# Kernel tuning notes

Hardware: AMD Instinct MI355X
Metric: run time of the kernel (lower is better)

Reference implementation:

```python
import jax, jax.numpy as jnp
import numpy as np

B, N, C, H, W = 4, 8, 256, 64, 64
SCALE = 2
D = C * SCALE  # embed_dim*scale, head_size with n_heads=1
EPS = 1e-6


def setup_inputs() -> dict:
    key = jax.random.key(0)
    ks = jax.random.split(key, 6)
    sc = lambda k, sh, f: jax.random.normal(k, sh, jnp.float32) * f
    return {
        "q": jax.random.normal(ks[0], (B, C), jnp.float32),
        "c": jax.random.normal(ks[1], (B, N, C, H, W), jnp.float32),
        "g": jnp.ones((C,), jnp.float32),                 # RMSNorm weight
        "Wq": sc(ks[2], (D, C), C ** -0.5),               # proj_q weight
        "Wkv": sc(ks[3], (2 * D, C), C ** -0.5),          # proj_kv weight
        "Wo": sc(ks[4], (C, D), D ** -0.5),               # proj_out weight
        "bo": jnp.zeros((C,), jnp.float32),               # proj_out bias
    }


def reference(q, c, g, Wq, Wkv, Wo, bo):
    # c: [B,N,C,H,W] -> [B,H,W,N,C]
    cp = jnp.transpose(c, (0, 3, 4, 1, 2))
    # RMSNorm over channel dim
    cn = cp * jax.lax.rsqrt(jnp.mean(cp * cp, axis=-1, keepdims=True) + EPS) * g
    # per-pixel, per-token k/v projection: [B,H,W,N,2D]
    kv = jnp.einsum('bhwnc,dc->bhwnd', cn, Wkv)
    k, v = jnp.split(kv, 2, axis=-1)                      # each [B,H,W,N,D]
    qp = q @ Wq.T                                         # [B,D]
    # broadcast single query over spatial grid; softmax over N context tokens
    dots = jnp.einsum('bd,bhwnd->bhwn', qp, k) * (D ** -0.5)
    att = jax.nn.softmax(dots, axis=-1)                   # [B,H,W,N]
    hvec = jnp.einsum('bhwn,bhwnd->bhwd', att, v)         # [B,H,W,D]
    out = hvec @ Wo.T + bo                                # [B,H,W,C]
    return jnp.transpose(out, (0, 3, 1, 2))               # [B,C,H,W]
```

## Files before the change

### kernel.cpp

```cpp
#include <hip/hip_runtime.h>


typedef __attribute__((ext_vector_type(8))) short short8;
typedef __attribute__((ext_vector_type(4))) float floatx4;

static __device__ __forceinline__ short f2bf(float f) {
  unsigned u = __float_as_uint(f);
  u += 0x7fffu + ((u >> 16) & 1u);
  return (short)(u >> 16);
}

__global__ __launch_bounds__(256) void pre_kernel(
    const float* __restrict__ q, const float* __restrict__ g,
    const float* __restrict__ Wq, const float* __restrict__ Wkv,
    const float* __restrict__ Wo, unsigned char* __restrict__ ws) {
  short* WovgB = (short*)ws;
  float* gqk = (float*)(ws + 131072);
  const int blk = blockIdx.x, tid = threadIdx.x;
  if (blk < 64) {
    const int i0 = blk * 4, c = tid;
    float s0 = 0.f, s1 = 0.f, s2 = 0.f, s3 = 0.f;
    #pragma unroll 8
    for (int d = 0; d < 512; ++d) {
      const float wv = Wkv[(512 + d) * 256 + c];
      s0 = fmaf(Wo[(i0 + 0) * 512 + d], wv, s0);
      s1 = fmaf(Wo[(i0 + 1) * 512 + d], wv, s1);
      s2 = fmaf(Wo[(i0 + 2) * 512 + d], wv, s2);
      s3 = fmaf(Wo[(i0 + 3) * 512 + d], wv, s3);
    }
    const float gc = g[c];
    const int sg = c >> 5, q2 = (c >> 3) & 3, jj = c & 7;
    const float sv[4] = {s0, s1, s2, s3};
    #pragma unroll
    for (int ii = 0; ii < 4; ++ii) {
      const int i = i0 + ii, it = i >> 4, m = i & 15;
      WovgB[((((it * 8 + sg) * 4 + q2) * 16) + m) * 8 + jj] = f2bf(sv[ii] * gc);
    }
  } else if (blk < 68) {
    const int b = blk - 64;
    __shared__ float qps[512];
    for (int d = tid; d < 512; d += 256) {
      float s = 0.f;
      #pragma unroll 16
      for (int cc = 0; cc < 256; ++cc)
        s = fmaf(Wq[d * 256 + cc], q[b * 256 + cc], s);
      qps[d] = s;
    }
    __syncthreads();
    const int c = tid;
    float s = 0.f;
    #pragma unroll 16
    for (int d = 0; d < 512; ++d)
      s = fmaf(Wkv[d * 256 + c], qps[d], s);
    gqk[b * 256 + c] = s * g[c] * 0.044194173824159216f;
  }
}

__global__ __launch_bounds__(512, 2) void attn_kernel(
    const float* __restrict__ cin, const float* __restrict__ bo,
    const unsigned char* __restrict__ ws, float* __restrict__ out) {
  const short8* Av = (const short8*)ws;
  const float* gqk = (const float*)(ws + 131072);
  const int blk = blockIdx.x;
  const int b = blk >> 6, h = blk & 63;
  const int tid = threadIdx.x;
  const int lane = tid & 63, w = tid >> 6;
  const int cgrp = tid >> 4;
  const int pgrp = tid & 15;

  __shared__ short tB[8][4][64][8];
  __shared__ float redS[2][8][16][4], redD[2][8][16][4];

  float rg[8];
  #pragma unroll
  for (int j = 0; j < 8; ++j) rg[j] = gqk[b * 256 + cgrp * 8 + j];

  float t[8][4];
  #pragma unroll
  for (int j = 0; j < 8; ++j)
    #pragma unroll
    for (int p = 0; p < 4; ++p) t[j][p] = 0.f;
  float mM[4], zZ[4];
  #pragma unroll
  for (int p = 0; p < 4; ++p) { mM[p] = -1e30f; zZ[p] = 0.f; }

  const float* cb = cin + ((size_t)(b * 8) * 256 + cgrp * 8) * 4096
                        + h * 64 + pgrp * 4;
  for (int n = 0; n < 8; ++n) {
    const float* cp = cb + (size_t)n * 256 * 4096;
    floatx4 vals[8];
    #pragma unroll
    for (int j = 0; j < 8; ++j)
      vals[j] = *(const floatx4*)(cp + (size_t)j * 4096);
    float ssq[4] = {0.f, 0.f, 0.f, 0.f}, dt[4] = {0.f, 0.f, 0.f, 0.f};
    #pragma unroll
    for (int j = 0; j < 8; ++j)
      #pragma unroll
      for (int p = 0; p < 4; ++p) {
        ssq[p] = fmaf(vals[j][p], vals[j][p], ssq[p]);
        dt[p] = fmaf(vals[j][p], rg[j], dt[p]);
      }
    #pragma unroll
    for (int p = 0; p < 4; ++p) {
      ssq[p] += __shfl_xor(ssq[p], 16);
      ssq[p] += __shfl_xor(ssq[p], 32);
      dt[p] += __shfl_xor(dt[p], 16);
      dt[p] += __shfl_xor(dt[p], 32);
    }
    if ((lane >> 4) == 0) {
      #pragma unroll
      for (int p = 0; p < 4; ++p) {
        redS[n & 1][w][pgrp][p] = ssq[p];
        redD[n & 1][w][pgrp][p] = dt[p];
      }
    }
    __syncthreads();
    floatx4 S = {0.f, 0.f, 0.f, 0.f}, Dt = {0.f, 0.f, 0.f, 0.f};
    #pragma unroll
    for (int ww = 0; ww < 8; ++ww) {
      S += *(const floatx4*)(&redS[n & 1][ww][pgrp][0]);
      Dt += *(const floatx4*)(&redD[n & 1][ww][pgrp][0]);
    }
    float wn[4], al[4];
    #pragma unroll
    for (int p = 0; p < 4; ++p) {
      const float invr = rsqrtf(S[p] * (1.f / 256.f) + 1e-6f);
      const float d = Dt[p] * invr;
      const float mn = fmaxf(mM[p], d);
      al[p] = __expf(mM[p] - mn);
      const float e = __expf(d - mn);
      zZ[p] = zZ[p] * al[p] + e;
      mM[p] = mn;
      wn[p] = e * invr;
    }
    #pragma unroll
    for (int j = 0; j < 8; ++j)
      #pragma unroll
      for (int p = 0; p < 4; ++p)
        t[j][p] = fmaf(wn[p], vals[j][p], t[j][p] * al[p]);
  }

  {
    const int s = cgrp >> 2, qq = cgrp & 3;
    const int nt = pgrp >> 2, mb = (pgrp & 3) * 4;
    #pragma unroll
    for (int p = 0; p < 4; ++p) {
      const float invZ = 1.f / zZ[p];
      short8 pk;
      #pragma unroll
      for (int j = 0; j < 8; ++j) pk[j] = f2bf(t[j][p] * invZ);
      *(short8*)(&tB[s][nt][qq * 16 + mb + p][0]) = pk;
    }
  }
  __syncthreads();

  const int qf = lane >> 4, m = lane & 15;
  floatx4 acc[2][4];
  #pragma unroll
  for (int mt = 0; mt < 2; ++mt)
    #pragma unroll
    for (int nt = 0; nt < 4; ++nt) acc[mt][nt] = (floatx4){0.f, 0.f, 0.f, 0.f};
  #pragma unroll
  for (int s = 0; s < 8; ++s) {
    short8 a[2];
    #pragma unroll
    for (int mt = 0; mt < 2; ++mt)
      a[mt] = Av[(((w * 2 + mt) * 8 + s) * 4 + qf) * 16 + m];
    #pragma unroll
    for (int nt = 0; nt < 4; ++nt) {
      const short8 bf = *(const short8*)(&tB[s][nt][lane][0]);
      #pragma unroll
      for (int mt = 0; mt < 2; ++mt)
        acc[mt][nt] = __builtin_amdgcn_mfma_f32_16x16x32_bf16(a[mt], bf, acc[mt][nt], 0, 0, 0);
    }
  }
  float* ob = out + (size_t)b * 256 * 4096 + h * 64;
  #pragma unroll
  for (int mt = 0; mt < 2; ++mt) {
    float bov[4];
    #pragma unroll
    for (int r = 0; r < 4; ++r) bov[r] = bo[(w * 2 + mt) * 16 + qf * 4 + r];
    #pragma unroll
    for (int nt = 0; nt < 4; ++nt)
      #pragma unroll
      for (int r = 0; r < 4; ++r) {
        const int i = (w * 2 + mt) * 16 + qf * 4 + r;
        ob[(size_t)i * 4096 + nt * 16 + m] = acc[mt][nt][r] + bov[r];
      }
  }
}

extern "C" void kernel_launch(void* const* d_in, const int* in_sizes, int n_in,
                              void* d_out, int out_size, void* d_ws, size_t ws_size,
                              hipStream_t stream) {
  const float* q   = (const float*)d_in[0];
  const float* c   = (const float*)d_in[1];
  const float* g   = (const float*)d_in[2];
  const float* Wq  = (const float*)d_in[3];
  const float* Wkv = (const float*)d_in[4];
  const float* Wo  = (const float*)d_in[5];
  const float* bo  = (const float*)d_in[6];
  float* out = (float*)d_out;
  unsigned char* ws = (unsigned char*)d_ws;
  pre_kernel<<<68, 256, 0, stream>>>(q, g, Wq, Wkv, Wo, ws);
  attn_kernel<<<256, 512, 0, stream>>>(c, bo, ws, out);
}
```

Measured before the change: 248.4 us.

## Split context tokens across blocks and move output projection to separate GEMM kernel

The attention kernel now splits the 8 context tokens into two halves and each row into two halves, launching 1024 smaller blocks instead of 256. Each block writes unnormalized bf16 partial sums and its running max/denominator to workspace. A new GEMM kernel merges the two halves with a softmax rescale, then applies the output projection with MFMA. This is meant to raise parallelism and occupancy on the memory-bound read of c. The cost is an extra kernel launch and a workspace round trip of about 16 MB of intermediates, plus extra bf16 rounding of the partials.

```diff
diff --git a/kernel.cpp b/kernel.cpp
--- a/kernel.cpp
+++ b/kernel.cpp
@@ -8,6 +8,9 @@
   unsigned u = __float_as_uint(f);
   u += 0x7fffu + ((u >> 16) & 1u);
   return (short)(u >> 16);
+}
+static __device__ __forceinline__ float bf2f(short s) {
+  return __uint_as_float(((unsigned)(unsigned short)s) << 16);
 }
 
 __global__ __launch_bounds__(256) void pre_kernel(
@@ -56,24 +59,22 @@
   }
 }
 
-__global__ __launch_bounds__(512, 2) void attn_kernel(
-    const float* __restrict__ cin, const float* __restrict__ bo,
-    const unsigned char* __restrict__ ws, float* __restrict__ out) {
-  const short8* Av = (const short8*)ws;
-  const float* gqk = (const float*)(ws + 131072);
+__global__ __launch_bounds__(256, 4) void attn_kernel(
+    const float* __restrict__ cin, const unsigned char* __restrict__ wsc,
+    unsigned char* __restrict__ ws) {
+  const float* gqk = (const float*)(wsc + 131072);
+  float2* mz = (float2*)(ws + 135168);
   const int blk = blockIdx.x;
-  const int b = blk >> 6, h = blk & 63;
+  const int b = blk >> 8, h = (blk >> 2) & 63, hf = (blk >> 1) & 1, nh = blk & 1;
   const int tid = threadIdx.x;
   const int lane = tid & 63, w = tid >> 6;
-  const int cgrp = tid >> 4;
-  const int pgrp = tid & 15;
-
-  __shared__ short tB[8][4][64][8];
-  __shared__ float redS[2][8][16][4], redD[2][8][16][4];
+  const int co = tid >> 3, pg = tid & 7;
+
+  __shared__ float redS[2][4][8][4], redD[2][4][8][4];
 
   float rg[8];
   #pragma unroll
-  for (int j = 0; j < 8; ++j) rg[j] = gqk[b * 256 + cgrp * 8 + j];
+  for (int j = 0; j < 8; ++j) rg[j] = gqk[b * 256 + co * 8 + j];
 
   float t[8][4];
   #pragma unroll
@@ -84,9 +85,9 @@
   #pragma unroll
   for (int p = 0; p < 4; ++p) { mM[p] = -1e30f; zZ[p] = 0.f; }
 
-  const float* cb = cin + ((size_t)(b * 8) * 256 + cgrp * 8) * 4096
-                        + h * 64 + pgrp * 4;
-  for (int n = 0; n < 8; ++n) {
+  const float* cb = cin + ((size_t)((b * 8 + nh * 4) * 256) + co * 8) * 4096
+                        + h * 64 + hf * 32 + pg * 4;
+  for (int n = 0; n < 4; ++n) {
     const float* cp = cb + (size_t)n * 256 * 4096;
     floatx4 vals[8];
     #pragma unroll
@@ -102,24 +103,26 @@
       }
     #pragma unroll
     for (int p = 0; p < 4; ++p) {
+      ssq[p] += __shfl_xor(ssq[p], 8);
       ssq[p] += __shfl_xor(ssq[p], 16);
       ssq[p] += __shfl_xor(ssq[p], 32);
+      dt[p] += __shfl_xor(dt[p], 8);
       dt[p] += __shfl_xor(dt[p], 16);
       dt[p] += __shfl_xor(dt[p], 32);
     }
-    if ((lane >> 4) == 0) {
+    if (lane < 8) {
       #pragma unroll
       for (int p = 0; p < 4; ++p) {
-        redS[n & 1][w][pgrp][p] = ssq[p];
-        redD[n & 1][w][pgrp][p] = dt[p];
+        redS[n & 1][w][pg][p] = ssq[p];
+        redD[n & 1][w][pg][p] = dt[p];
       }
     }
     __syncthreads();
     floatx4 S = {0.f, 0.f, 0.f, 0.f}, Dt = {0.f, 0.f, 0.f, 0.f};
     #pragma unroll
-    for (int ww = 0; ww < 8; ++ww) {
-      S += *(const floatx4*)(&redS[n & 1][ww][pgrp][0]);
-      Dt += *(const floatx4*)(&redD[n & 1][ww][pgrp][0]);
+    for (int ww = 0; ww < 4; ++ww) {
+      S += *(const floatx4*)(&redS[n & 1][ww][pg][0]);
+      Dt += *(const floatx4*)(&redD[n & 1][ww][pg][0]);
     }
     float wn[4], al[4];
     #pragma unroll
@@ -141,53 +144,84 @@
   }
 
   {
-    const int s = cgrp >> 2, qq = cgrp & 3;
-    const int nt = pgrp >> 2, mb = (pgrp & 3) * 4;
+    short8* te = (short8*)(ws + 397312 + (size_t)nh * 8388608);
+    const int s = co >> 2, qq = co & 3;
+    const int P = h * 4 + hf * 2 + (pg >> 2), mb = (pg & 3) * 4;
     #pragma unroll
     for (int p = 0; p < 4; ++p) {
-      const float invZ = 1.f / zZ[p];
       short8 pk;
       #pragma unroll
-      for (int j = 0; j < 8; ++j) pk[j] = f2bf(t[j][p] * invZ);
-      *(short8*)(&tB[s][nt][qq * 16 + mb + p][0]) = pk;
-    }
+      for (int j = 0; j < 8; ++j) pk[j] = f2bf(t[j][p]);
+      te[(((b * 256 + P) * 8 + s) * 4 + qq) * 16 + mb + p] = pk;
+    }
+  }
+  if (tid < 8) {
+    const int px = h * 64 + hf * 32 + pg * 4;
+    #pragma unroll
+    for (int p = 0; p < 4; ++p)
+      mz[((size_t)(nh * 4 + b)) * 4096 + px + p] = make_float2(mM[p], zZ[p]);
+  }
+}
+
+__global__ __launch_bounds__(256, 2) void gemm_kernel(
+    const float* __restrict__ bo, const unsigned char* __restrict__ ws,
+    float* __restrict__ out) {
+  const short8* Av = (const short8*)ws;
+  const float2* mz = (const float2*)(ws + 135168);
+  const short8* T1 = (const short8*)(ws + 397312);
+  const short8* T2 = (const short8*)(ws + 8785920);
+  __shared__ short8 tBs[1024];
+  __shared__ float2 ff[256];
+  const int blk = blockIdx.x, tid = threadIdx.x;
+  const int b = blk >> 6, ig = (blk >> 4) & 3, pxg = blk & 15;
+  const int lane = tid & 63, w = tid >> 6;
+  const int it = ig * 4 + w;
+  const int qf = lane >> 4, m = lane & 15;
+
+  {
+    const int px = pxg * 256 + tid;
+    const float2 a = mz[(size_t)b * 4096 + px];
+    const float2 c2 = mz[(size_t)(4 + b) * 4096 + px];
+    const float M = fmaxf(a.x, c2.x);
+    const float s1 = __expf(a.x - M), s2 = __expf(c2.x - M);
+    const float den = 1.f / (s1 * a.y + s2 * c2.y);
+    ff[tid] = make_float2(s1 * den, s2 * den);
   }
   __syncthreads();
 
-  const int qf = lane >> 4, m = lane & 15;
-  floatx4 acc[2][4];
-  #pragma unroll
-  for (int mt = 0; mt < 2; ++mt)
-    #pragma unroll
-    for (int nt = 0; nt < 4; ++nt) acc[mt][nt] = (floatx4){0.f, 0.f, 0.f, 0.f};
+  floatx4 acc[16];
+  #pragma unroll
+  for (int nt = 0; nt < 16; ++nt) acc[nt] = (floatx4){0.f, 0.f, 0.f, 0.f};
   #pragma unroll
   for (int s = 0; s < 8; ++s) {
-    short8 a[2];
-    #pragma unroll
-    for (int mt = 0; mt < 2; ++mt)
-      a[mt] = Av[(((w * 2 + mt) * 8 + s) * 4 + qf) * 16 + m];
-    #pragma unroll
-    for (int nt = 0; nt < 4; ++nt) {
-      const short8 bf = *(const short8*)(&tB[s][nt][lane][0]);
-      #pragma unroll
-      for (int mt = 0; mt < 2; ++mt)
-        acc[mt][nt] = __builtin_amdgcn_mfma_f32_16x16x32_bf16(a[mt], bf, acc[mt][nt], 0, 0, 0);
-    }
-  }
-  float* ob = out + (size_t)b * 256 * 4096 + h * 64;
-  #pragma unroll
-  for (int mt = 0; mt < 2; ++mt) {
-    float bov[4];
-    #pragma unroll
-    for (int r = 0; r < 4; ++r) bov[r] = bo[(w * 2 + mt) * 16 + qf * 4 + r];
-    #pragma unroll
-    for (int nt = 0; nt < 4; ++nt)
-      #pragma unroll
-      for (int r = 0; r < 4; ++r) {
-        const int i = (w * 2 + mt) * 16 + qf * 4 + r;
-        ob[(size_t)i * 4096 + nt * 16 + m] = acc[mt][nt][r] + bov[r];
-      }
-  }
+    if (s) __syncthreads();
+    #pragma unroll
+    for (int k = 0; k < 4; ++k) {
+      const int idx = tid + k * 256;
+      const int nt = idx >> 6, r = idx & 63;
+      const size_t src = (size_t)((b * 256 + pxg * 16 + nt) * 8 + s) * 64 + r;
+      const short8 v1 = T1[src], v2 = T2[src];
+      const float2 f = ff[nt * 16 + (r & 15)];
+      short8 mg;
+      #pragma unroll
+      for (int j = 0; j < 8; ++j)
+        mg[j] = f2bf(f.x * bf2f(v1[j]) + f.y * bf2f(v2[j]));
+      tBs[idx] = mg;
+    }
+    __syncthreads();
+    const short8 a = Av[((it * 8 + s) * 4 + qf) * 16 + m];
+    #pragma unroll
+    for (int nt = 0; nt < 16; ++nt)
+      acc[nt] = __builtin_amdgcn_mfma_f32_16x16x32_bf16(a, tBs[nt * 64 + lane], acc[nt], 0, 0, 0);
+  }
+  float* ob = out + (size_t)(b * 256) * 4096 + pxg * 256;
+  #pragma unroll
+  for (int nt = 0; nt < 16; ++nt)
+    #pragma unroll
+    for (int r = 0; r < 4; ++r) {
+      const int i = it * 16 + qf * 4 + r;
+      ob[(size_t)i * 4096 + nt * 16 + m] = acc[nt][r] + bo[i];
+    }
 }
 
 extern "C" void kernel_launch(void* const* d_in, const int* in_sizes, int n_in,
@@ -203,5 +237,6 @@
   float* out = (float*)d_out;
   unsigned char* ws = (unsigned char*)d_ws;
   pre_kernel<<<68, 256, 0, stream>>>(q, g, Wq, Wkv, Wo, ws);
-  attn_kernel<<<256, 512, 0, stream>>>(c, bo, ws, out);
-}
+  attn_kernel<<<1024, 256, 0, stream>>>(c, ws, ws);
+  gemm_kernel<<<256, 256, 0, stream>>>(bo, ws, out);
+}
```

New measurement: 298.9 us. 1.2x slower.
